# Kernel optimization log

Measured on AMD Instinct MI355X. Metric: run time of the kernel, lower is better.

The kernel has to match this reference:

```python
import jax, jax.numpy as jnp
import numpy as np

B, T, C, H, W = 2, 2048, 2048, 16, 512
D = C // H  # head_dim = 128

def setup_inputs() -> dict:
    key = jax.random.key(0)
    k1, k2, k3 = jax.random.split(key, 3)
    x = jax.random.normal(k1, (B, T, C), dtype=jnp.float32)
    w_attn = jax.random.normal(k2, (C, 3 * C), dtype=jnp.float32) * 0.02
    w_proj = jax.random.normal(k3, (C, C), dtype=jnp.float32) * 0.02
    # standard RoPE tables: [T, D] with halves repeated
    inv_freq = 1.0 / (10000.0 ** (jnp.arange(0, D, 2, dtype=jnp.float32) / D))
    freqs = jnp.outer(jnp.arange(T, dtype=jnp.float32), inv_freq)  # [T, D/2]
    emb = jnp.concatenate([freqs, freqs], axis=-1)  # [T, D]
    return {"x": x, "freqs_cos": jnp.cos(emb), "freqs_sin": jnp.sin(emb),
            "w_attn": w_attn, "w_proj": w_proj}

def _rotate_half(t):
    return jnp.concatenate([-t[..., D // 2:], t[..., :D // 2]], axis=-1)

def reference(x, freqs_cos, freqs_sin, w_attn, w_proj):
    qkv = x @ w_attn  # [B,T,3C]
    q, k, v = jnp.split(qkv, 3, axis=-1)
    # [B,T,C] -> [B,H,T,D]
    q = q.reshape(B, T, H, D).transpose(0, 2, 1, 3)
    k = k.reshape(B, T, H, D).transpose(0, 2, 1, 3)
    v = v.reshape(B, T, H, D).transpose(0, 2, 1, 3)
    cos = freqs_cos[None, None, :, :]  # [1,1,T,D]
    sin = freqs_sin[None, None, :, :]
    q = q * cos + _rotate_half(q) * sin
    k = k * cos + _rotate_half(k) * sin
    scores = jnp.einsum('bhqd,bhkd->bhqk', q, k) / jnp.sqrt(jnp.float32(D))
    i = jnp.arange(T)[:, None]
    j = jnp.arange(T)[None, :]
    band = (j <= i) & (j > i - W)  # causal sliding window of width W
    scores = jnp.where(band[None, None, :, :], scores, -jnp.inf)
    att = jax.nn.softmax(scores, axis=-1)
    y = jnp.einsum('bhqk,bhkd->bhqd', att, v)
    y = y.transpose(0, 2, 1, 3).reshape(B, T, C)
    return y @ w_proj
```

## Files before the change

kernel.cpp:

```cpp
#include <hip/hip_runtime.h>
#include <stdint.h>

#define B_ 2
#define T_ 2048
#define C_ 2048
#define H_ 16
#define D_ 128
#define W_ 512
#define M_ (B_*T_)
#define N1_ (3*C_)

typedef short bf16x8 __attribute__((ext_vector_type(8)));
typedef unsigned short u16x8 __attribute__((ext_vector_type(8)));
typedef float f32x4 __attribute__((ext_vector_type(4)));

#define SB() __builtin_amdgcn_sched_barrier(0)

__device__ __forceinline__ unsigned short f2bf(float f) {
  union { float f; unsigned u; } v; v.f = f;
  unsigned r = v.u + 0x7fffu + ((v.u >> 16) & 1u);
  return (unsigned short)(r >> 16);
}
__device__ __forceinline__ float bf2f(unsigned short b) {
  union { unsigned u; float f; } v; v.u = ((unsigned)b) << 16;
  return v.f;
}

__device__ __forceinline__ void gload_lds16(const void* g, void* l) {
  __builtin_amdgcn_global_load_lds((const __attribute__((address_space(1))) void*)g,
                                   (__attribute__((address_space(3))) void*)l, 16, 0, 0);
}

__global__ void k_cvt(const float* __restrict__ s, unsigned short* __restrict__ d, int n) {
  int i = (blockIdx.x * blockDim.x + threadIdx.x) * 8;
  if (i >= n) return;
  float4 a = *(const float4*)(s + i);
  float4 b = *(const float4*)(s + i + 4);
  u16x8 o;
  o[0]=f2bf(a.x); o[1]=f2bf(a.y); o[2]=f2bf(a.z); o[3]=f2bf(a.w);
  o[4]=f2bf(b.x); o[5]=f2bf(b.y); o[6]=f2bf(b.z); o[7]=f2bf(b.w);
  *(u16x8*)(d + i) = o;
}

__global__ void k_tcvt(const float* __restrict__ s, unsigned short* __restrict__ d, int R, int Cc) {
  __shared__ float tile[32][33];
  int c0 = blockIdx.x * 32, r0 = blockIdx.y * 32;
  int tx = threadIdx.x & 31, ty = threadIdx.x >> 5;
  #pragma unroll
  for (int j = 0; j < 32; j += 8) tile[ty + j][tx] = s[(size_t)(r0 + ty + j) * Cc + c0 + tx];
  __syncthreads();
  #pragma unroll
  for (int j = 0; j < 32; j += 8) d[(size_t)(c0 + ty + j) * R + r0 + tx] = f2bf(tile[tx][ty + j]);
}

template<int ROWS, int K>
__device__ __forceinline__ void stage_half(const unsigned short* __restrict__ gbase,
                                           int row0, int kt, int kh,
                                           unsigned short* region, int tid, int sw) {
  const char* gsrc = (const char*)(gbase + (size_t)row0 * K + kt * 64 + kh * 32);
  {
    int o = tid * 16, s = o ^ sw;
    gload_lds16(gsrc + (size_t)(s >> 6) * (K * 2) + (s & 63), (char*)region + o);
  }
  if (ROWS == 256) {
    int o = (512 + tid) * 16, s = o ^ sw;
    gload_lds16(gsrc + (size_t)(s >> 6) * (K * 2) + (s & 63), (char*)region + o);
  }
}

template<int K, int Ntot>
__global__ __launch_bounds__(512, 2) void k_gemmF(const unsigned short* __restrict__ A,
                                                  const unsigned short* __restrict__ Bt,
                                                  const float* __restrict__ fcos,
                                                  const float* __restrict__ fsin,
                                                  unsigned short* __restrict__ q_r,
                                                  unsigned short* __restrict__ k_r,
                                                  unsigned short* __restrict__ vq) {
  __shared__ unsigned short As[2][2][256 * 32];
  __shared__ unsigned short Bs[2][2][256 * 32];
  const int tid = threadIdx.x, lane = tid & 63, wv = tid >> 6;
  const int wm = wv >> 2, wn = wv & 3;
  const int lr = lane & 15, lg = lane >> 4;
  const int sw = tid & 32;
  const int fofs = lr * 64 + ((lg * 16) ^ ((lr & 8) << 2));
  const int aoff = wm * 128 * 64 + fofs;
  int bofs[4];
  #pragma unroll
  for (int j = 0; j < 4; ++j)
    bofs[j] = ((wn >> 1) * 128 + (wn & 1) * 32 + (j >> 1) * 64 + (j & 1) * 16) * 64 + fofs;

  const int nwg = gridDim.x;
  const int nbx = Ntot >> 8;
  const int q = nwg >> 3, r = nwg & 7;
  const int xcd = blockIdx.x & 7, off = blockIdx.x >> 3;
  const int bid = (xcd < r ? xcd * (q + 1) : r * (q + 1) + (xcd - r) * q) + off;
  const int bm0 = (bid / nbx) << 8;
  const int bn0 = (bid % nbx) << 8;

  f32x4 acc[8][4];
  #pragma unroll
  for (int i = 0; i < 8; ++i)
    #pragma unroll
    for (int j = 0; j < 4; ++j)
      #pragma unroll
      for (int e = 0; e < 4; ++e) acc[i][j][e] = 0.f;

  constexpr int NT = K >> 6;

  stage_half<256, K>(A,  bm0, 0, 0, As[0][0], tid, sw);
  stage_half<256, K>(Bt, bn0, 0, 0, Bs[0][0], tid, sw);
  stage_half<256, K>(Bt, bn0, 0, 1, Bs[0][1], tid, sw);
  stage_half<256, K>(A,  bm0, 0, 1, As[0][1], tid, sw);
  stage_half<256, K>(Bt, bn0, 1, 0, Bs[1][0], tid, sw);
  stage_half<256, K>(A,  bm0, 1, 0, As[1][0], tid, sw);
  stage_half<256, K>(Bt, bn0, 1, 1, Bs[1][1], tid, sw);
  asm volatile("s_waitcnt vmcnt(4)" ::: "memory");
  __builtin_amdgcn_s_barrier();

  bf16x8 Xa[4], Xb[4], Ya[4];
  #pragma unroll
  for (int j = 0; j < 4; ++j) Xb[j] = *(const bf16x8*)((const char*)Bs[0][0] + bofs[j]);
  #pragma unroll
  for (int i = 0; i < 4; ++i) Xa[i] = *(const bf16x8*)((const char*)As[0][0] + aoff + i * 1024);

  #pragma unroll 2
  for (int t = 0; t < NT; ++t) {
    const int p = t & 1;
    asm volatile("s_waitcnt lgkmcnt(0)" ::: "memory");
    SB();
    __builtin_amdgcn_s_setprio(1);
    #pragma unroll
    for (int i = 0; i < 4; ++i)
      #pragma unroll
      for (int j = 0; j < 4; ++j)
        acc[i][j] = __builtin_amdgcn_mfma_f32_16x16x32_bf16(Xa[i], Xb[j], acc[i][j], 0, 0, 0);
    __builtin_amdgcn_s_setprio(0);
    #pragma unroll
    for (int i = 0; i < 4; ++i) Ya[i] = *(const bf16x8*)((const char*)As[p][0] + aoff + (i + 4) * 1024);
    if (t + 1 < NT) stage_half<256, K>(A, bm0, t + 1, 1, As[p ^ 1][1], tid, sw);
    __builtin_amdgcn_s_barrier();

    asm volatile("s_waitcnt lgkmcnt(0)" ::: "memory");
    SB();
    __builtin_amdgcn_s_setprio(1);
    #pragma unroll
    for (int i = 0; i < 4; ++i)
      #pragma unroll
      for (int j = 0; j < 4; ++j)
        acc[i + 4][j] = __builtin_amdgcn_mfma_f32_16x16x32_bf16(Ya[i], Xb[j], acc[i + 4][j], 0, 0, 0);
    __builtin_amdgcn_s_setprio(0);
    #pragma unroll
    for (int j = 0; j < 4; ++j) Xb[j] = *(const bf16x8*)((const char*)Bs[p][1] + bofs[j]);
    #pragma unroll
    for (int i = 0; i < 4; ++i) Xa[i] = *(const bf16x8*)((const char*)As[p][1] + aoff + i * 1024);
    if (t + 2 < NT) stage_half<256, K>(Bt, bn0, t + 2, 0, Bs[p][0], tid, sw);
    __builtin_amdgcn_s_barrier();

    asm volatile("s_waitcnt lgkmcnt(0)" ::: "memory");
    SB();
    __builtin_amdgcn_s_setprio(1);
    #pragma unroll
    for (int i = 0; i < 4; ++i)
      #pragma unroll
      for (int j = 0; j < 4; ++j)
        acc[i][j] = __builtin_amdgcn_mfma_f32_16x16x32_bf16(Xa[i], Xb[j], acc[i][j], 0, 0, 0);
    __builtin_amdgcn_s_setprio(0);
    #pragma unroll
    for (int i = 0; i < 4; ++i) Ya[i] = *(const bf16x8*)((const char*)As[p][1] + aoff + (i + 4) * 1024);
    if (t + 2 < NT) stage_half<256, K>(A, bm0, t + 2, 0, As[p][0], tid, sw);
    __builtin_amdgcn_s_barrier();

    asm volatile("s_waitcnt lgkmcnt(0)" ::: "memory");
    SB();
    __builtin_amdgcn_s_setprio(1);
    #pragma unroll
    for (int i = 0; i < 4; ++i)
      #pragma unroll
      for (int j = 0; j < 4; ++j)
        acc[i + 4][j] = __builtin_amdgcn_mfma_f32_16x16x32_bf16(Ya[i], Xb[j], acc[i + 4][j], 0, 0, 0);
    __builtin_amdgcn_s_setprio(0);
    if (t < NT - 2) asm volatile("s_waitcnt vmcnt(4)" ::: "memory");
    else            asm volatile("s_waitcnt vmcnt(0)" ::: "memory");
    #pragma unroll
    for (int j = 0; j < 4; ++j) Xb[j] = *(const bf16x8*)((const char*)Bs[p ^ 1][0] + bofs[j]);
    #pragma unroll
    for (int i = 0; i < 4; ++i) Xa[i] = *(const bf16x8*)((const char*)As[p ^ 1][0] + aoff + i * 1024);
    if (t + 2 < NT) stage_half<256, K>(Bt, bn0, t + 2, 1, Bs[p][1], tid, sw);
    __builtin_amdgcn_s_barrier();
  }
  asm volatile("s_waitcnt lgkmcnt(0)" ::: "memory");

  const int nb  = bn0 >> 11;
  const int rem = bn0 & 2047;
  const int b   = bm0 >> 11;
  const int t0  = bm0 & 2047;
  const int wcb = (wn >> 1) * 128 + (wn & 1) * 32;

  if (nb == 2) {
    #pragma unroll
    for (int i = 0; i < 8; ++i)
      #pragma unroll
      for (int j = 0; j < 4; ++j) {
        int col = rem + wcb + (j >> 1) * 64 + (j & 1) * 16 + lr;
        #pragma unroll
        for (int e = 0; e < 4; ++e) {
          int t = t0 + wm * 128 + i * 16 + lg * 4 + e;
          vq[((size_t)(b * T_ + t)) * C_ + col] = f2bf(acc[i][j][e]);
        }
      }
  } else {
    unsigned short* dst = nb ? k_r : q_r;
    #pragma unroll
    for (int i = 0; i < 8; ++i)
      #pragma unroll
      for (int j = 0; j < 4; ++j) {
        int col = rem + wcb + (j >> 1) * 64 + (j & 1) * 16 + lr;
        int head = col >> 7, d = col & 127;
        float sgn = (j < 2) ? -1.f : 1.f;
        #pragma unroll
        for (int e = 0; e < 4; ++e) {
          int t = t0 + wm * 128 + i * 16 + lg * 4 + e;
          float c = fcos[t * D_ + d];
          float s = fsin[t * D_ + d];
          float out = acc[i][j][e] * c + sgn * acc[i][j ^ 2][e] * s;
          dst[((size_t)(b * H_ + head) * T_ + t) * D_ + d] = f2bf(out);
        }
      }
  }
}

template<int K, int Ntot>
__global__ __launch_bounds__(512, 4) void k_gemmS(const unsigned short* __restrict__ A,
                                                  const unsigned short* __restrict__ Bt,
                                                  float* __restrict__ Cp) {
  __shared__ unsigned short As[2][2][128 * 32];
  __shared__ unsigned short Bs[2][2][128 * 32];
  const int tid = threadIdx.x, lane = tid & 63, wv = tid >> 6;
  const int wm = wv >> 1, wn = wv & 1;
  const int lr = lane & 15, lg = lane >> 4;
  const int sw = tid & 32;
  const int fofs = lr * 64 + ((lg * 16) ^ ((lr & 8) << 2));
  const int aoff = wm * 32 * 64 + fofs;
  const int boff = wn * 64 * 64 + fofs;

  const int nwg = gridDim.x;
  const int nbx = Ntot >> 7;
  const int q = nwg >> 3, r = nwg & 7;
  const int xcd = blockIdx.x & 7, off = blockIdx.x >> 3;
  const int bid = (xcd < r ? xcd * (q + 1) : r * (q + 1) + (xcd - r) * q) + off;
  const int bm0 = (bid / nbx) << 7;
  const int bn0 = (bid % nbx) << 7;

  f32x4 acc[2][4];
  #pragma unroll
  for (int i = 0; i < 2; ++i)
    #pragma unroll
    for (int j = 0; j < 4; ++j)
      #pragma unroll
      for (int e = 0; e < 4; ++e) acc[i][j][e] = 0.f;

  constexpr int NT = K >> 6;

  auto stage_tile = [&](int kt, int rr) {
    stage_half<128, K>(A,  bm0, kt, 0, As[rr][0], tid, sw);
    stage_half<128, K>(Bt, bn0, kt, 0, Bs[rr][0], tid, sw);
    stage_half<128, K>(A,  bm0, kt, 1, As[rr][1], tid, sw);
    stage_half<128, K>(Bt, bn0, kt, 1, Bs[rr][1], tid, sw);
  };

  stage_tile(0, 0);
  asm volatile("s_waitcnt vmcnt(0)" ::: "memory");
  __builtin_amdgcn_s_barrier();

  for (int t = 0; t < NT; ++t) {
    const int p = t & 1;
    if (t + 1 < NT) stage_tile(t + 1, p ^ 1);

    bf16x8 af[2], bfr[4];
    #pragma unroll
    for (int kh = 0; kh < 2; ++kh) {
      #pragma unroll
      for (int i = 0; i < 2; ++i) af[i] = *(const bf16x8*)((const char*)As[p][kh] + aoff + i * 1024);
      #pragma unroll
      for (int j = 0; j < 4; ++j) bfr[j] = *(const bf16x8*)((const char*)Bs[p][kh] + boff + j * 1024);
      asm volatile("s_waitcnt lgkmcnt(0)" ::: "memory");
      SB();
      __builtin_amdgcn_s_setprio(1);
      #pragma unroll
      for (int i = 0; i < 2; ++i)
        #pragma unroll
        for (int j = 0; j < 4; ++j)
          acc[i][j] = __builtin_amdgcn_mfma_f32_16x16x32_bf16(af[i], bfr[j], acc[i][j], 0, 0, 0);
      __builtin_amdgcn_s_setprio(0);
    }
    asm volatile("s_waitcnt vmcnt(0)" ::: "memory");
    __builtin_amdgcn_s_barrier();
  }

  #pragma unroll
  for (int i = 0; i < 2; ++i)
    #pragma unroll
    for (int j = 0; j < 4; ++j) {
      int m = bm0 + wm * 32 + i * 16 + lg * 4;
      int n = bn0 + wn * 64 + j * 16 + lr;
      #pragma unroll
      for (int e = 0; e < 4; ++e)
        Cp[(size_t)(m + e) * Ntot + n] = acc[i][j][e];
    }
}

__global__ __launch_bounds__(256) void k_vt(const unsigned short* __restrict__ vq,
                                            unsigned short* __restrict__ v_t) {
  const int bh = blockIdx.x, b = bh >> 4, h = bh & 15;
  const int t0 = blockIdx.y * 64;
  const int tid = threadIdx.x;
  __shared__ unsigned short vt[64][136];
  #pragma unroll
  for (int p = 0; p < 4; ++p) {
    int idx = p * 256 + tid;
    int tl = idx >> 4, sg = idx & 15;
    int t = t0 + tl, d0 = sg * 8;
    *(u16x8*)&vt[tl][d0] = *(const u16x8*)(vq + (size_t)(b*T_ + t) * C_ + h*D_ + d0);
  }
  __syncthreads();
  #pragma unroll
  for (int p = 0; p < 4; ++p) {
    int idx = p * 256 + tid;
    int sg = idx & 7, d = idx >> 3;
    u16x8 o;
    #pragma unroll
    for (int e = 0; e < 8; ++e) o[e] = vt[sg*8 + e][d];
    *(u16x8*)(v_t + (size_t)((b*H_ + h)*D_ + d) * T_ + t0 + sg*8) = o;
  }
}

__global__ __launch_bounds__(512) void k_attn(const unsigned short* __restrict__ q_r,
                       const unsigned short* __restrict__ k_r,
                       const unsigned short* __restrict__ v_t,
                       unsigned short* __restrict__ y) {
  const int bh = blockIdx.x, b = bh >> 4, h = bh & 15;
  const int q0 = blockIdx.y * 128;
  const int tid = threadIdx.x, lane = tid & 63, wv = tid >> 6;
  const int lr = lane & 15, lg = lane >> 4;

  __shared__ unsigned short Ks[2][64 * 128];
  __shared__ unsigned short Vs[128 * 64];
  __shared__ unsigned short Ps[8 * 16 * 64];

  const size_t bhT = (size_t)(b*H_ + h) * T_;
  const size_t bhD = (size_t)(b*H_ + h) * D_;
  const unsigned short* qbase = q_r + (bhT + q0 + wv*16 + lr) * D_;
  bf16x8 qf[4];
  #pragma unroll
  for (int kk = 0; kk < 4; ++kk) qf[kk] = *(const bf16x8*)(qbase + kk*32 + lg*8);

  f32x4 o[8];
  #pragma unroll
  for (int i = 0; i < 8; ++i)
    #pragma unroll
    for (int e = 0; e < 4; ++e) o[i][e] = 0.f;
  float m_run[4], l_sum[4];
  #pragma unroll
  for (int e = 0; e < 4; ++e) { m_run[e] = -1e30f; l_sum[e] = 0.f; }

  const int i_min = q0 + wv*16, i_max = i_min + 15;
  int kt_lo = q0 - (W_ - 1); if (kt_lo < 0) kt_lo = 0; kt_lo &= ~63;
  const float scale = 0.08838834764831845f;

  unsigned short* Ps_w = Ps + wv * 1024;

  auto stage_k = [&](int kt, int buf) {
    #pragma unroll
    for (int c = 0; c < 2; ++c) {
      int ob = (c * 512 + tid) * 16;
      int row = ob >> 8, slot = (ob >> 4) & 15;
      int cb = slot ^ ((row & 7) << 1);
      gload_lds16(k_r + (bhT + kt + row) * D_ + cb * 8, (char*)Ks[buf] + ob);
    }
  };
  auto stage_v = [&](int kt) {
    #pragma unroll
    for (int c = 0; c < 2; ++c) {
      int ob = (c * 512 + tid) * 16;
      int d = ob >> 7, slot = (ob >> 4) & 7;
      int cb = slot ^ (d & 7);
      gload_lds16(v_t + (bhD + d) * T_ + kt + cb * 8, (char*)Vs + ob);
    }
  };

  stage_k(kt_lo, 0);
  int cur = 0;
  for (int kt = kt_lo; kt < q0 + 128; kt += 64) {
    const bool has_next = (kt + 64 < q0 + 128);
    stage_v(kt);
    if (has_next) stage_k(kt + 64, cur ^ 1);
    if (has_next) asm volatile("s_waitcnt vmcnt(2)" ::: "memory");
    else          asm volatile("s_waitcnt vmcnt(0)" ::: "memory");
    __builtin_amdgcn_s_barrier();

    const bool live = (kt <= i_max) && (kt + 63 >= i_min - (W_ - 1));
    float sv[4][4];
    if (live) {
      const unsigned short* Kc = Ks[cur];
      f32x4 s[4];
      #pragma unroll
      for (int ct = 0; ct < 4; ++ct)
        #pragma unroll
        for (int e = 0; e < 4; ++e) s[ct][e] = 0.f;
      #pragma unroll
      for (int kk = 0; kk < 4; ++kk) {
        #pragma unroll
        for (int ct = 0; ct < 4; ++ct) {
          bf16x8 kf = *(const bf16x8*)&Kc[(ct*16 + lr)*128 + ((kk*4 + lg) ^ ((lr & 7) << 1))*8];
          s[ct] = __builtin_amdgcn_mfma_f32_16x16x32_bf16(qf[kk], kf, s[ct], 0, 0, 0);
        }
      }
      float mnew[4];
      int grow = 0;
      #pragma unroll
      for (int e = 0; e < 4; ++e) {
        int i = i_min + lg*4 + e;
        float rm = -1e30f;
        #pragma unroll
        for (int ct = 0; ct < 4; ++ct) {
          int j = kt + ct*16 + lr;
          bool ok = (j <= i) && (j > i - W_);
          sv[e][ct] = ok ? s[ct][e] * scale : -1e30f;
          rm = fmaxf(rm, sv[e][ct]);
        }
        #pragma unroll
        for (int msk = 1; msk < 16; msk <<= 1) rm = fmaxf(rm, __shfl_xor(rm, msk));
        mnew[e] = fmaxf(m_run[e], rm);
        grow |= (mnew[e] > m_run[e]) ? 1 : 0;
      }
      if (__any(grow)) {
        #pragma unroll
        for (int e = 0; e < 4; ++e) {
          float fac = __expf(m_run[e] - mnew[e]);
          l_sum[e] *= fac;
          m_run[e] = mnew[e];
          #pragma unroll
          for (int nt = 0; nt < 8; ++nt) o[nt][e] *= fac;
        }
      }
      #pragma unroll
      for (int e = 0; e < 4; ++e) {
        int prow = lg*4 + e;
        float rs = 0.f;
        #pragma unroll
        for (int ct = 0; ct < 4; ++ct) {
          float pv = (sv[e][ct] > -1e29f) ? __expf(sv[e][ct] - m_run[e]) : 0.f;
          rs += pv;
          Ps_w[prow*64 + ((ct*2 + (lr >> 3)) ^ (prow & 7))*8 + (lr & 7)] = f2bf(pv);
        }
        #pragma unroll
        for (int msk = 1; msk < 16; msk <<= 1) rs += __shfl_xor(rs, msk);
        l_sum[e] += rs;
      }
      asm volatile("s_waitcnt lgkmcnt(0)" ::: "memory"); SB();
      #pragma unroll
      for (int kk = 0; kk < 2; ++kk) {
        bf16x8 pf = *(const bf16x8*)&Ps_w[lr*64 + ((kk*4 + lg) ^ (lr & 7))*8];
        #pragma unroll
        for (int nt = 0; nt < 8; ++nt) {
          bf16x8 vf = *(const bf16x8*)&Vs[(nt*16 + lr)*64 + ((kk*4 + lg) ^ (lr & 7))*8];
          o[nt] = __builtin_amdgcn_mfma_f32_16x16x32_bf16(pf, vf, o[nt], 0, 0, 0);
        }
      }
    }
    asm volatile("s_waitcnt lgkmcnt(0)" ::: "memory");
    __builtin_amdgcn_s_barrier();
    cur ^= 1;
  }

  #pragma unroll
  for (int nt = 0; nt < 8; ++nt) {
    #pragma unroll
    for (int e = 0; e < 4; ++e) {
      int t = q0 + wv*16 + lg*4 + e;
      int d = nt*16 + lr;
      y[(size_t)(b*T_ + t) * C_ + h*D_ + d] = f2bf(o[nt][e] / l_sum[e]);
    }
  }
}

extern "C" void kernel_launch(void* const* d_in, const int* in_sizes, int n_in,
                              void* d_out, int out_size, void* d_ws, size_t ws_size,
                              hipStream_t stream) {
  const float* x      = (const float*)d_in[0];
  const float* fcos   = (const float*)d_in[1];
  const float* fsin   = (const float*)d_in[2];
  const float* w_attn = (const float*)d_in[3];
  const float* w_proj = (const float*)d_in[4];
  float* out = (float*)d_out;

  char* ws = (char*)d_ws;
  unsigned short* x_bf = (unsigned short*)(ws);
  unsigned short* wa_t = (unsigned short*)(ws + 16777216ull);
  unsigned short* wp_t = (unsigned short*)(ws + 41943040ull);
  unsigned short* vq   = (unsigned short*)(ws + 50331648ull);
  unsigned short* q_r  = (unsigned short*)(ws + 100663296ull);
  unsigned short* k_r  = (unsigned short*)(ws + 117440512ull);
  unsigned short* v_t  = (unsigned short*)(ws + 134217728ull);
  unsigned short* y_bf = x_bf;

  k_cvt<<<dim3(4096), dim3(256), 0, stream>>>(x, x_bf, M_*C_);
  k_tcvt<<<dim3(192, 64), dim3(256), 0, stream>>>(w_attn, wa_t, C_, N1_);
  k_tcvt<<<dim3(64, 64), dim3(256), 0, stream>>>(w_proj, wp_t, C_, C_);
  k_gemmF<C_, N1_><<<dim3(384), dim3(512), 0, stream>>>(x_bf, wa_t, fcos, fsin, q_r, k_r, vq);
  k_vt<<<dim3(32, 32), dim3(256), 0, stream>>>(vq, v_t);
  k_attn<<<dim3(32, 16), dim3(512), 0, stream>>>(q_r, k_r, v_t, y_bf);
  k_gemmS<C_, C_><<<dim3(512), dim3(512), 0, stream>>>(y_bf, wp_t, out);
}
```

Baseline: 266.1 us.

## Split-K the tail tiles of the QKV GEMM to balance the wave

The QKV projection has 384 tiles of 256x256. The first 256 tiles still go through the fused GEMM with the RoPE epilogue. The remaining 128 tiles are each split into two K-halves run by separate blocks, giving 256 blocks, so both launches fill the device evenly instead of leaving a partial second wave. The partial sums are written as bf16 into a workspace buffer and into the output buffer, then a new epilogue kernel adds them and applies RoPE or the V copy. This adds an extra launch and extra memory traffic, and storing partials in bf16 loses some precision.

```diff
diff --git a/kernel.cpp b/kernel.cpp
--- a/kernel.cpp
+++ b/kernel.cpp
@@ -230,6 +230,179 @@
 }
 
 template<int K, int Ntot>
+__global__ __launch_bounds__(512, 2) void k_gemmH(const unsigned short* __restrict__ A,
+                                                  const unsigned short* __restrict__ Bt,
+                                                  unsigned short* __restrict__ p0,
+                                                  unsigned short* __restrict__ p1) {
+  __shared__ unsigned short As[2][2][256 * 32];
+  __shared__ unsigned short Bs[2][2][256 * 32];
+  const int tid = threadIdx.x, lane = tid & 63, wv = tid >> 6;
+  const int wm = wv >> 2, wn = wv & 3;
+  const int lr = lane & 15, lg = lane >> 4;
+  const int sw = tid & 32;
+  const int fofs = lr * 64 + ((lg * 16) ^ ((lr & 8) << 2));
+  const int aoff = wm * 128 * 64 + fofs;
+  const int boff = wn * 64 * 64 + fofs;
+
+  const int nwg = gridDim.x;
+  const int q = nwg >> 3, r = nwg & 7;
+  const int xcd = blockIdx.x & 7, off = blockIdx.x >> 3;
+  const int bid = (xcd < r ? xcd * (q + 1) : r * (q + 1) + (xcd - r) * q) + off;
+  const int tl = bid >> 1, half = bid & 1;
+  const int tile = 256 + tl;
+  const int bm0 = (tile / 24) << 8;
+  const int bn0 = (tile % 24) << 8;
+  const int koff = half * 16;
+  unsigned short* pp = half ? p1 : p0;
+
+  f32x4 acc[8][4];
+  #pragma unroll
+  for (int i = 0; i < 8; ++i)
+    #pragma unroll
+    for (int j = 0; j < 4; ++j)
+      #pragma unroll
+      for (int e = 0; e < 4; ++e) acc[i][j][e] = 0.f;
+
+  constexpr int NT = 16;
+
+  stage_half<256, K>(A,  bm0, koff + 0, 0, As[0][0], tid, sw);
+  stage_half<256, K>(Bt, bn0, koff + 0, 0, Bs[0][0], tid, sw);
+  stage_half<256, K>(Bt, bn0, koff + 0, 1, Bs[0][1], tid, sw);
+  stage_half<256, K>(A,  bm0, koff + 0, 1, As[0][1], tid, sw);
+  stage_half<256, K>(Bt, bn0, koff + 1, 0, Bs[1][0], tid, sw);
+  stage_half<256, K>(A,  bm0, koff + 1, 0, As[1][0], tid, sw);
+  stage_half<256, K>(Bt, bn0, koff + 1, 1, Bs[1][1], tid, sw);
+  asm volatile("s_waitcnt vmcnt(4)" ::: "memory");
+  __builtin_amdgcn_s_barrier();
+
+  bf16x8 Xa[4], Xb[4], Ya[4];
+  #pragma unroll
+  for (int j = 0; j < 4; ++j) Xb[j] = *(const bf16x8*)((const char*)Bs[0][0] + boff + j * 1024);
+  #pragma unroll
+  for (int i = 0; i < 4; ++i) Xa[i] = *(const bf16x8*)((const char*)As[0][0] + aoff + i * 1024);
+
+  #pragma unroll 2
+  for (int t = 0; t < NT; ++t) {
+    const int p = t & 1;
+    asm volatile("s_waitcnt lgkmcnt(0)" ::: "memory");
+    SB();
+    __builtin_amdgcn_s_setprio(1);
+    #pragma unroll
+    for (int i = 0; i < 4; ++i)
+      #pragma unroll
+      for (int j = 0; j < 4; ++j)
+        acc[i][j] = __builtin_amdgcn_mfma_f32_16x16x32_bf16(Xa[i], Xb[j], acc[i][j], 0, 0, 0);
+    __builtin_amdgcn_s_setprio(0);
+    #pragma unroll
+    for (int i = 0; i < 4; ++i) Ya[i] = *(const bf16x8*)((const char*)As[p][0] + aoff + (i + 4) * 1024);
+    if (t + 1 < NT) stage_half<256, K>(A, bm0, koff + t + 1, 1, As[p ^ 1][1], tid, sw);
+    __builtin_amdgcn_s_barrier();
+
+    asm volatile("s_waitcnt lgkmcnt(0)" ::: "memory");
+    SB();
+    __builtin_amdgcn_s_setprio(1);
+    #pragma unroll
+    for (int i = 0; i < 4; ++i)
+      #pragma unroll
+      for (int j = 0; j < 4; ++j)
+        acc[i + 4][j] = __builtin_amdgcn_mfma_f32_16x16x32_bf16(Ya[i], Xb[j], acc[i + 4][j], 0, 0, 0);
+    __builtin_amdgcn_s_setprio(0);
+    #pragma unroll
+    for (int j = 0; j < 4; ++j) Xb[j] = *(const bf16x8*)((const char*)Bs[p][1] + boff + j * 1024);
+    #pragma unroll
+    for (int i = 0; i < 4; ++i) Xa[i] = *(const bf16x8*)((const char*)As[p][1] + aoff + i * 1024);
+    if (t + 2 < NT) stage_half<256, K>(Bt, bn0, koff + t + 2, 0, Bs[p][0], tid, sw);
+    __builtin_amdgcn_s_barrier();
+
+    asm volatile("s_waitcnt lgkmcnt(0)" ::: "memory");
+    SB();
+    __builtin_amdgcn_s_setprio(1);
+    #pragma unroll
+    for (int i = 0; i < 4; ++i)
+      #pragma unroll
+      for (int j = 0; j < 4; ++j)
+        acc[i][j] = __builtin_amdgcn_mfma_f32_16x16x32_bf16(Xa[i], Xb[j], acc[i][j], 0, 0, 0);
+    __builtin_amdgcn_s_setprio(0);
+    #pragma unroll
+    for (int i = 0; i < 4; ++i) Ya[i] = *(const bf16x8*)((const char*)As[p][1] + aoff + (i + 4) * 1024);
+    if (t + 2 < NT) stage_half<256, K>(A, bm0, koff + t + 2, 0, As[p][0], tid, sw);
+    __builtin_amdgcn_s_barrier();
+
+    asm volatile("s_waitcnt lgkmcnt(0)" ::: "memory");
+    SB();
+    __builtin_amdgcn_s_setprio(1);
+    #pragma unroll
+    for (int i = 0; i < 4; ++i)
+      #pragma unroll
+      for (int j = 0; j < 4; ++j)
+        acc[i + 4][j] = __builtin_amdgcn_mfma_f32_16x16x32_bf16(Ya[i], Xb[j], acc[i + 4][j], 0, 0, 0);
+    __builtin_amdgcn_s_setprio(0);
+    if (t < NT - 2) asm volatile("s_waitcnt vmcnt(4)" ::: "memory");
+    else            asm volatile("s_waitcnt vmcnt(0)" ::: "memory");
+    #pragma unroll
+    for (int j = 0; j < 4; ++j) Xb[j] = *(const bf16x8*)((const char*)Bs[p ^ 1][0] + boff + j * 1024);
+    #pragma unroll
+    for (int i = 0; i < 4; ++i) Xa[i] = *(const bf16x8*)((const char*)As[p ^ 1][0] + aoff + i * 1024);
+    if (t + 2 < NT) stage_half<256, K>(Bt, bn0, koff + t + 2, 1, Bs[p][1], tid, sw);
+    __builtin_amdgcn_s_barrier();
+  }
+  asm volatile("s_waitcnt lgkmcnt(0)" ::: "memory");
+
+  #pragma unroll
+  for (int i = 0; i < 8; ++i)
+    #pragma unroll
+    for (int j = 0; j < 4; ++j) {
+      int ml = wm * 128 + i * 16 + lg * 4;
+      int nl = wn * 64 + j * 16 + lr;
+      #pragma unroll
+      for (int e = 0; e < 4; ++e)
+        pp[(size_t)tl * 65536 + (ml + e) * 256 + nl] = f2bf(acc[i][j][e]);
+    }
+}
+
+__global__ __launch_bounds__(256) void k_epi(const unsigned short* __restrict__ p0,
+                                             const unsigned short* __restrict__ p1,
+                                             const float* __restrict__ fcos,
+                                             const float* __restrict__ fsin,
+                                             unsigned short* __restrict__ q_r,
+                                             unsigned short* __restrict__ k_r,
+                                             unsigned short* __restrict__ vq) {
+  int g = blockIdx.x * 256 + threadIdx.x;
+  int tl = g >> 13, ml = (g >> 5) & 255, nl0 = (g & 31) * 8;
+  int tile = 256 + tl;
+  int bm0 = (tile / 24) << 8, bn0 = (tile % 24) << 8;
+  size_t base = (size_t)tl * 65536 + (size_t)ml * 256;
+  u16x8 a0 = *(const u16x8*)(p0 + base + nl0);
+  u16x8 a1 = *(const u16x8*)(p1 + base + nl0);
+  int col0 = bn0 + nl0;
+  int nb = col0 >> 11;
+  int b = bm0 >> 11, t = (bm0 & 2047) + ml;
+  if (nb == 2) {
+    u16x8 o;
+    #pragma unroll
+    for (int e = 0; e < 8; ++e) o[e] = f2bf(bf2f(a0[e]) + bf2f(a1[e]));
+    *(u16x8*)(vq + (size_t)(b * T_ + t) * C_ + (col0 & 2047)) = o;
+  } else {
+    u16x8 b0 = *(const u16x8*)(p0 + base + (nl0 ^ 64));
+    u16x8 b1 = *(const u16x8*)(p1 + base + (nl0 ^ 64));
+    int lc = col0 & 2047;
+    int head = lc >> 7, d0 = lc & 127;
+    float sgn = (d0 & 64) ? 1.f : -1.f;
+    u16x8 o;
+    #pragma unroll
+    for (int e = 0; e < 8; ++e) {
+      float c = fcos[t * D_ + d0 + e];
+      float s = fsin[t * D_ + d0 + e];
+      float self = bf2f(a0[e]) + bf2f(a1[e]);
+      float pr   = bf2f(b0[e]) + bf2f(b1[e]);
+      o[e] = f2bf(self * c + sgn * pr * s);
+    }
+    unsigned short* dst = nb ? k_r : q_r;
+    *(u16x8*)(dst + ((size_t)(b * H_ + head) * T_ + t) * D_ + d0) = o;
+  }
+}
+
+template<int K, int Ntot>
 __global__ __launch_bounds__(512, 4) void k_gemmS(const unsigned short* __restrict__ A,
                                                   const unsigned short* __restrict__ Bt,
                                                   float* __restrict__ Cp) {
@@ -499,6 +672,8 @@
   unsigned short* wa_t = (unsigned short*)(ws + 16777216ull);
   unsigned short* wp_t = (unsigned short*)(ws + 41943040ull);
   unsigned short* vq   = (unsigned short*)(ws + 50331648ull);
+  unsigned short* p0   = (unsigned short*)(ws + 67108864ull);
+  unsigned short* p1   = (unsigned short*)d_out;
   unsigned short* q_r  = (unsigned short*)(ws + 100663296ull);
   unsigned short* k_r  = (unsigned short*)(ws + 117440512ull);
   unsigned short* v_t  = (unsigned short*)(ws + 134217728ull);
@@ -507,7 +682,9 @@
   k_cvt<<<dim3(4096), dim3(256), 0, stream>>>(x, x_bf, M_*C_);
   k_tcvt<<<dim3(192, 64), dim3(256), 0, stream>>>(w_attn, wa_t, C_, N1_);
   k_tcvt<<<dim3(64, 64), dim3(256), 0, stream>>>(w_proj, wp_t, C_, C_);
-  k_gemmF<C_, N1_><<<dim3(384), dim3(512), 0, stream>>>(x_bf, wa_t, fcos, fsin, q_r, k_r, vq);
+  k_gemmF<C_, N1_><<<dim3(256), dim3(512), 0, stream>>>(x_bf, wa_t, fcos, fsin, q_r, k_r, vq);
+  k_gemmH<C_, N1_><<<dim3(256), dim3(512), 0, stream>>>(x_bf, wa_t, p0, p1);
+  k_epi<<<dim3(4096), dim3(256), 0, stream>>>(p0, p1, fcos, fsin, q_r, k_r, vq);
   k_vt<<<dim3(32, 32), dim3(256), 0, stream>>>(vq, v_t);
   k_attn<<<dim3(32, 16), dim3(512), 0, stream>>>(q_r, k_r, v_t, y_bf);
   k_gemmS<C_, C_><<<dim3(512), dim3(512), 0, stream>>>(y_bf, wp_t, out);
```

New measurement: 269.0 us. Within noise of the previous version (+1.1%).
